# Kernel tuning notes

Hardware: AMD Instinct MI355X
Metric: run time of the kernel (lower is better)

The kernel has to match this reference:

```python
import jax, jax.numpy as jnp
import numpy as np

N_POINTS = 131072
N_SEG = 16
C = 256
BN_EPS = 1e-5


def setup_inputs() -> dict:
    key = jax.random.key(0)
    ks = jax.random.split(key, 6)
    x = jax.random.normal(ks[0], (N_POINTS, C), jnp.float32)
    # Ragged segment end-offsets (cumulative counts), strictly increasing, last == N_POINTS.
    rng = np.random.default_rng(0)
    base = N_POINTS // N_SEG
    counts = base + rng.integers(-base // 32, base // 32, N_SEG)
    counts[-1] += N_POINTS - counts.sum()
    o = jnp.asarray(np.cumsum(counts), jnp.int32)
    s1 = 1.0 / np.sqrt(2 * C)  # linear1: Linear(2C -> C)
    s2 = 1.0 / np.sqrt(C)      # linear2: Linear(C -> C)
    W1 = jax.random.uniform(ks[1], (2 * C, C), jnp.float32, -s1, s1)
    b1 = jax.random.uniform(ks[2], (C,), jnp.float32, -s1, s1)
    W2 = jax.random.uniform(ks[3], (C, C), jnp.float32, -s2, s2)
    b2 = jax.random.uniform(ks[4], (C,), jnp.float32, -s2, s2)
    gamma = jnp.ones((C,), jnp.float32)
    beta = jnp.zeros((C,), jnp.float32)
    return {"x": x, "o": o, "W1": W1, "b1": b1, "W2": W2, "b2": b2,
            "gamma": gamma, "beta": beta}


def reference(x, o, W1, b1, W2, b2, gamma, beta):
    n, c = x.shape
    s = o.shape[0]
    # segment id per point from cumulative end-offsets
    seg_id = jnp.searchsorted(o, jnp.arange(n), side="right")  # [N]
    counts = jnp.concatenate([o[:1], o[1:] - o[:-1]])          # [S]
    # per-segment mean pooling (x_b.sum(0, True) / cnt)
    sums = jax.ops.segment_sum(x, seg_id, num_segments=s)      # [S, C]
    means = sums / counts[:, None].astype(x.dtype)
    # linear2: Linear(C, C) + ReLU on segment means
    y = jax.nn.relu(means @ W2 + b2)                           # [S, C]
    # broadcast-concat back to points, then linear1: Linear(2C, C)
    h = jnp.concatenate([x, y[seg_id]], axis=1) @ W1 + b1      # [N, C]
    # BatchNorm1d (training mode: batch statistics, biased variance) + ReLU
    mu = h.mean(axis=0)
    var = h.var(axis=0)
    out = jax.nn.relu((h - mu) * (gamma / jnp.sqrt(var + BN_EPS)) + beta)
    return out
```

## Files before the change

kernel.cpp:

```cpp
#include <hip/hip_runtime.h>
#include <stdint.h>

#define N_PTS 131072
#define NC 256
#define NSEG 16
#define BN_EPSF 1e-5f

typedef __attribute__((ext_vector_type(8))) short bf16x8;
typedef __attribute__((ext_vector_type(4))) float f32x4;

__device__ __forceinline__ unsigned short f2bf(float f) {
  union { float f; uint32_t u; } v; v.f = f;
  uint32_t u = v.u;
  uint32_t r = (u + 0x7fffu + ((u >> 16) & 1u)) >> 16;
  return (unsigned short)r;
}

__device__ __forceinline__ int swz(int col, int row) {
  return (col & ~63) | ((((col >> 3) & 7) ^ (row & 7)) << 3) | (col & 7);
}

__device__ __forceinline__ void gll16(const unsigned short* g, unsigned short* l) {
  __builtin_amdgcn_global_load_lds(
      (const __attribute__((address_space(1))) void*)g,
      (__attribute__((address_space(3))) void*)l, 16, 0, 0);
}

__global__ __launch_bounds__(256) void k_prep(const float* __restrict__ W1,
                                              unsigned short* __restrict__ w1t,
                                              float* __restrict__ zerobuf) {
  int b = blockIdx.x, t = threadIdx.x;
  if (b >= 16) {
    int i = (b - 16) * 256 + t;
    if (i < 8448) zerobuf[i] = 0.f;
    return;
  }
  __shared__ float tile[64][65];
  int bx = b & 3, by = b >> 2;
  int k0 = by * 64, j0 = bx * 64;
  int r = t >> 6, c = t & 63;
#pragma unroll
  for (int i = 0; i < 16; ++i) {
    int kk = r + i * 4;
    tile[kk][c] = W1[(size_t)(k0 + kk) * NC + j0 + c];
  }
  __syncthreads();
#pragma unroll
  for (int i = 0; i < 16; ++i) {
    int jj = r + i * 4;
    int row = j0 + jj, col = k0 + c;
    w1t[(size_t)row * NC + swz(col, row)] = f2bf(tile[c][jj]);
  }
}

__global__ __launch_bounds__(256) void k_gemm1(
    const float* __restrict__ x, const int* __restrict__ o,
    const unsigned short* __restrict__ w1t,
    unsigned short* __restrict__ x_bf,
    float* __restrict__ seg_sums, float* __restrict__ hseg,
    float* __restrict__ gsumsq) {
  __shared__ __align__(16) unsigned short lA[64 * NC];
  __shared__ __align__(16) unsigned short lB[NC * 64];
  __shared__ float s_acc[2][NC];
  __shared__ float s_hA[NC], s_hB[NC], s_q[NC];
  __shared__ int o_s[NSEG];
  int t = threadIdx.x, lane = t & 63, w = t >> 6;
  int row0 = blockIdx.x * 64;
  if (t < NSEG) o_s[t] = o[t];
  s_acc[0][t] = 0.f;
  s_acc[1][t] = 0.f;
  __syncthreads();
  int c0 = lane * 4;
  int s0 = 0;
  while (o_s[s0] <= row0) ++s0;
  int e0 = o_s[s0];
  int s1 = (s0 < NSEG - 1) ? s0 + 1 : s0;

  {
    float4 accA = {0.f, 0.f, 0.f, 0.f}, accB = {0.f, 0.f, 0.f, 0.f};
    const float4* xv = (const float4*)x;
#pragma unroll
    for (int i = 0; i < 16; ++i) {
      int rl = w + i * 4;
      int r = row0 + rl;
      float4 v = xv[(size_t)r * 64 + lane];
      ushort4 b;
      b.x = f2bf(v.x); b.y = f2bf(v.y); b.z = f2bf(v.z); b.w = f2bf(v.w);
      int sc = swz(c0, r);
      *(ushort4*)(x_bf + (size_t)r * NC + sc) = b;
      *(ushort4*)(lA + rl * NC + sc) = b;
      bool inA = (r < e0);
      accA.x += inA ? v.x : 0.f; accB.x += inA ? 0.f : v.x;
      accA.y += inA ? v.y : 0.f; accB.y += inA ? 0.f : v.y;
      accA.z += inA ? v.z : 0.f; accB.z += inA ? 0.f : v.z;
      accA.w += inA ? v.w : 0.f; accB.w += inA ? 0.f : v.w;
    }
    atomicAdd(&s_acc[0][c0 + 0], accA.x);
    atomicAdd(&s_acc[0][c0 + 1], accA.y);
    atomicAdd(&s_acc[0][c0 + 2], accA.z);
    atomicAdd(&s_acc[0][c0 + 3], accA.w);
    atomicAdd(&s_acc[1][c0 + 0], accB.x);
    atomicAdd(&s_acc[1][c0 + 1], accB.y);
    atomicAdd(&s_acc[1][c0 + 2], accB.z);
    atomicAdd(&s_acc[1][c0 + 3], accB.w);
  }

  f32x4 acc[4][4] = {};
  for (int kt = 0; kt < 4; ++kt) {
#pragma unroll
    for (int i = 0; i < 8; ++i) {
      int tp = t + i * 256;
      gll16(w1t + (size_t)(tp >> 3) * NC + kt * 64 + (t & 7) * 8, lB + tp * 8);
    }
    __syncthreads();
#pragma unroll
    for (int kk = 0; kk < 2; ++kk) {
      bf16x8 af[4], bfr[4];
      int sl = kk * 4 + (lane >> 4);
#pragma unroll
      for (int mm = 0; mm < 4; ++mm) {
        int r = mm * 16 + (lane & 15);
        af[mm] = *(const bf16x8*)(lA + r * NC + kt * 64 + ((sl ^ (r & 7)) << 3));
      }
#pragma unroll
      for (int nn = 0; nn < 4; ++nn) {
        int jrow = w * 64 + nn * 16 + (lane & 15);
        bfr[nn] = *(const bf16x8*)(lB + jrow * 64 + ((sl ^ (jrow & 7)) << 3));
      }
#pragma unroll
      for (int mm = 0; mm < 4; ++mm)
#pragma unroll
        for (int nn = 0; nn < 4; ++nn)
          acc[mm][nn] = __builtin_amdgcn_mfma_f32_16x16x32_bf16(af[mm], bfr[nn],
                                                                acc[mm][nn], 0, 0, 0);
    }
    __syncthreads();
  }

  int cl = lane & 15, q = lane >> 4;
#pragma unroll
  for (int nn = 0; nn < 4; ++nn) {
    int col = w * 64 + nn * 16 + cl;
    float pA = 0.f, pB = 0.f, pq = 0.f;
#pragma unroll
    for (int mm = 0; mm < 4; ++mm) {
#pragma unroll
      for (int r_ = 0; r_ < 4; ++r_) {
        int row = row0 + mm * 16 + q * 4 + r_;
        float gv = acc[mm][nn][r_];
        bool inA = (row < e0);
        pA += inA ? gv : 0.f;
        pB += inA ? 0.f : gv;
        pq += gv * gv;
      }
    }
    pA += __shfl_xor(pA, 16, 64); pA += __shfl_xor(pA, 32, 64);
    pB += __shfl_xor(pB, 16, 64); pB += __shfl_xor(pB, 32, 64);
    pq += __shfl_xor(pq, 16, 64); pq += __shfl_xor(pq, 32, 64);
    if (q == 0) { s_hA[col] = pA; s_hB[col] = pB; s_q[col] = pq; }
  }
  __syncthreads();
  atomicAdd(&seg_sums[s0 * NC + t], s_acc[0][t]);
  atomicAdd(&seg_sums[s1 * NC + t], s_acc[1][t]);
  atomicAdd(&hseg[s0 * NC + t], s_hA[t]);
  atomicAdd(&hseg[s1 * NC + t], s_hB[t]);
  atomicAdd(&gsumsq[t], s_q[t]);
}

__global__ __launch_bounds__(256) void k_seg_mlp(
    const int* __restrict__ o, const float* __restrict__ seg_sums,
    const float* __restrict__ W1, const float* __restrict__ b1,
    const float* __restrict__ W2, const float* __restrict__ b2,
    float* __restrict__ z) {
  __shared__ float mean_s[NC];
  __shared__ float y_s[NC];
  int b = blockIdx.x, j = threadIdx.x;
  int start = (b == 0) ? 0 : o[b - 1];
  float inv = 1.f / (float)(o[b] - start);
  mean_s[j] = seg_sums[b * NC + j] * inv;
  __syncthreads();
  float a = b2[j];
  for (int k = 0; k < NC; ++k) a += mean_s[k] * W2[k * NC + j];
  y_s[j] = fmaxf(a, 0.f);
  __syncthreads();
  float a2 = b1[j];
  for (int k = 0; k < NC; ++k) a2 += y_s[k] * W1[(NC + k) * NC + j];
  z[b * NC + j] = a2;
}

__global__ __launch_bounds__(256) void k_gemm2(
    const unsigned short* __restrict__ x_bf, const unsigned short* __restrict__ w1t,
    const int* __restrict__ o, const float* __restrict__ z,
    const float* __restrict__ hseg, const float* __restrict__ gsumsq,
    const float* __restrict__ gamma, const float* __restrict__ beta,
    float* __restrict__ out) {
  __shared__ __align__(16) unsigned short lA[64 * NC];
  __shared__ __align__(16) unsigned short lB[NC * 64];
  __shared__ float s_scale[NC], s_shift[NC];
  __shared__ int o_s[NSEG];
  int t = threadIdx.x, lane = t & 63, w = t >> 6;
  int row0 = blockIdx.x * 64;
  if (t < NSEG) o_s[t] = o[t];
  __syncthreads();
  {
    float cs = 0.f, cq = gsumsq[t];
    int prev = 0;
#pragma unroll
    for (int s = 0; s < NSEG; ++s) {
      float cnt = (float)(o_s[s] - prev);
      prev = o_s[s];
      float hs = hseg[s * NC + t], zz = z[s * NC + t];
      cs += hs + cnt * zz;
      cq += (2.f * hs + cnt * zz) * zz;
    }
    float invN = 1.f / (float)N_PTS;
    float mu = cs * invN;
    float var = cq * invN - mu * mu;
    float sc = gamma[t] * rsqrtf(var + BN_EPSF);
    s_scale[t] = sc;
    s_shift[t] = beta[t] - mu * sc;
  }
#pragma unroll
  for (int i = 0; i < 8; ++i) {
    int tp = t + i * 256;
    gll16(x_bf + (size_t)(row0 + (tp >> 5)) * NC + (tp & 31) * 8, lA + tp * 8);
  }
  f32x4 acc[4][4] = {};
  for (int kt = 0; kt < 4; ++kt) {
#pragma unroll
    for (int i = 0; i < 8; ++i) {
      int tp = t + i * 256;
      gll16(w1t + (size_t)(tp >> 3) * NC + kt * 64 + (t & 7) * 8, lB + tp * 8);
    }
    __syncthreads();
#pragma unroll
    for (int kk = 0; kk < 2; ++kk) {
      bf16x8 af[4], bfr[4];
      int sl = kk * 4 + (lane >> 4);
#pragma unroll
      for (int mm = 0; mm < 4; ++mm) {
        int r = mm * 16 + (lane & 15);
        af[mm] = *(const bf16x8*)(lA + r * NC + kt * 64 + ((sl ^ (r & 7)) << 3));
      }
#pragma unroll
      for (int nn = 0; nn < 4; ++nn) {
        int jrow = w * 64 + nn * 16 + (lane & 15);
        bfr[nn] = *(const bf16x8*)(lB + jrow * 64 + ((sl ^ (jrow & 7)) << 3));
      }
#pragma unroll
      for (int mm = 0; mm < 4; ++mm)
#pragma unroll
        for (int nn = 0; nn < 4; ++nn)
          acc[mm][nn] = __builtin_amdgcn_mfma_f32_16x16x32_bf16(bfr[nn], af[mm],
                                                                acc[mm][nn], 0, 0, 0);
    }
    __syncthreads();
  }
  int s0 = 0;
  while (o_s[s0] <= row0) ++s0;
  int e0 = o_s[s0];
  int s1 = (s0 < NSEG - 1) ? s0 + 1 : s0;
  int rl = lane & 15, q = lane >> 4;
#pragma unroll
  for (int mm = 0; mm < 4; ++mm) {
    int row = row0 + mm * 16 + rl;
    int sg = (row < e0) ? s0 : s1;
#pragma unroll
    for (int nn = 0; nn < 4; ++nn) {
      int c = w * 64 + nn * 16 + q * 4;
      float4 z4 = *(const float4*)(z + sg * NC + c);
      float4 sc4 = *(const float4*)(s_scale + c);
      float4 sh4 = *(const float4*)(s_shift + c);
      float4 o4;
      o4.x = fmaxf((acc[mm][nn][0] + z4.x) * sc4.x + sh4.x, 0.f);
      o4.y = fmaxf((acc[mm][nn][1] + z4.y) * sc4.y + sh4.y, 0.f);
      o4.z = fmaxf((acc[mm][nn][2] + z4.z) * sc4.z + sh4.z, 0.f);
      o4.w = fmaxf((acc[mm][nn][3] + z4.w) * sc4.w + sh4.w, 0.f);
      *(float4*)(out + (size_t)row * NC + c) = o4;
    }
  }
}

extern "C" void kernel_launch(void* const* d_in, const int* in_sizes, int n_in,
                              void* d_out, int out_size, void* d_ws, size_t ws_size,
                              hipStream_t stream) {
  const float* x = (const float*)d_in[0];
  const int* o = (const int*)d_in[1];
  const float* W1 = (const float*)d_in[2];
  const float* b1 = (const float*)d_in[3];
  const float* W2 = (const float*)d_in[4];
  const float* b2 = (const float*)d_in[5];
  const float* gamma = (const float*)d_in[6];
  const float* beta = (const float*)d_in[7];
  float* out = (float*)d_out;

  char* ws = (char*)d_ws;
  unsigned short* x_bf = (unsigned short*)ws;
  char* base2 = ws + 67108864;
  float* seg_sums = (float*)(base2);
  float* hseg     = (float*)(base2 + 16384);
  float* gsumsq   = (float*)(base2 + 32768);
  float* z        = (float*)(base2 + 33792);
  unsigned short* w1t = (unsigned short*)(base2 + 50176);

  k_prep<<<49, 256, 0, stream>>>(W1, w1t, seg_sums);
  k_gemm1<<<2048, 256, 0, stream>>>(x, o, w1t, x_bf, seg_sums, hseg, gsumsq);
  k_seg_mlp<<<16, 256, 0, stream>>>(o, seg_sums, W1, b1, W2, b2, z);
  k_gemm2<<<2048, 256, 0, stream>>>(x_bf, w1t, o, z, hseg, gsumsq,
                                    gamma, beta, out);
}
```

Before: 346.5 us.

## Store GEMM1 result in bf16 and replace second GEMM with elementwise apply

Instead of writing bf16 x and recomputing the x@W1 GEMM in a second kernel, the first GEMM now stores its output tile as bf16 to workspace, and the final kernel only reads it back, adds the segment term and applies BatchNorm and ReLU. GEMM1 moves to 512 threads per block, with each wave covering 32 columns, and issues the first W1 k-tile load before the x conversion. This removes a whole second GEMM and its W1 tile loads, at the cost of rounding the pre-BN activation to bf16 before normalisation, which may add numerical error.

```diff
diff --git a/kernel.cpp b/kernel.cpp
--- a/kernel.cpp
+++ b/kernel.cpp
@@ -14,6 +14,9 @@
   uint32_t u = v.u;
   uint32_t r = (u + 0x7fffu + ((u >> 16) & 1u)) >> 16;
   return (unsigned short)r;
+}
+__device__ __forceinline__ float bf2f(unsigned short h) {
+  union { uint32_t u; float f; } v; v.u = ((uint32_t)h) << 16; return v.f;
 }
 
 __device__ __forceinline__ int swz(int col, int row) {
@@ -53,10 +56,10 @@
   }
 }
 
-__global__ __launch_bounds__(256) void k_gemm1(
+__global__ __launch_bounds__(512, 4) void k_gemm1(
     const float* __restrict__ x, const int* __restrict__ o,
     const unsigned short* __restrict__ w1t,
-    unsigned short* __restrict__ x_bf,
+    unsigned short* __restrict__ g_bf,
     float* __restrict__ seg_sums, float* __restrict__ hseg,
     float* __restrict__ gsumsq) {
   __shared__ __align__(16) unsigned short lA[64 * NC];
@@ -67,9 +70,15 @@
   int t = threadIdx.x, lane = t & 63, w = t >> 6;
   int row0 = blockIdx.x * 64;
   if (t < NSEG) o_s[t] = o[t];
-  s_acc[0][t] = 0.f;
-  s_acc[1][t] = 0.f;
-  __syncthreads();
+  if (t < NC) { s_acc[0][t] = 0.f; s_acc[1][t] = 0.f; }
+  __syncthreads();
+
+#pragma unroll
+  for (int i = 0; i < 4; ++i) {
+    int tp = t + i * 512;
+    gll16(w1t + (size_t)(tp >> 3) * NC + (tp & 7) * 8, lB + tp * 8);
+  }
+
   int c0 = lane * 4;
   int s0 = 0;
   while (o_s[s0] <= row0) ++s0;
@@ -80,15 +89,13 @@
     float4 accA = {0.f, 0.f, 0.f, 0.f}, accB = {0.f, 0.f, 0.f, 0.f};
     const float4* xv = (const float4*)x;
 #pragma unroll
-    for (int i = 0; i < 16; ++i) {
-      int rl = w + i * 4;
+    for (int i = 0; i < 8; ++i) {
+      int rl = w + i * 8;
       int r = row0 + rl;
       float4 v = xv[(size_t)r * 64 + lane];
       ushort4 b;
       b.x = f2bf(v.x); b.y = f2bf(v.y); b.z = f2bf(v.z); b.w = f2bf(v.w);
-      int sc = swz(c0, r);
-      *(ushort4*)(x_bf + (size_t)r * NC + sc) = b;
-      *(ushort4*)(lA + rl * NC + sc) = b;
+      *(ushort4*)(lA + rl * NC + swz(c0, rl)) = b;
       bool inA = (r < e0);
       accA.x += inA ? v.x : 0.f; accB.x += inA ? 0.f : v.x;
       accA.y += inA ? v.y : 0.f; accB.y += inA ? 0.f : v.y;
@@ -105,17 +112,19 @@
     atomicAdd(&s_acc[1][c0 + 3], accB.w);
   }
 
-  f32x4 acc[4][4] = {};
+  f32x4 acc[4][2] = {};
   for (int kt = 0; kt < 4; ++kt) {
-#pragma unroll
-    for (int i = 0; i < 8; ++i) {
-      int tp = t + i * 256;
-      gll16(w1t + (size_t)(tp >> 3) * NC + kt * 64 + (t & 7) * 8, lB + tp * 8);
+    if (kt > 0) {
+#pragma unroll
+      for (int i = 0; i < 4; ++i) {
+        int tp = t + i * 512;
+        gll16(w1t + (size_t)(tp >> 3) * NC + kt * 64 + (tp & 7) * 8, lB + tp * 8);
+      }
     }
     __syncthreads();
 #pragma unroll
     for (int kk = 0; kk < 2; ++kk) {
-      bf16x8 af[4], bfr[4];
+      bf16x8 af[4], bfr[2];
       int sl = kk * 4 + (lane >> 4);
 #pragma unroll
       for (int mm = 0; mm < 4; ++mm) {
@@ -123,48 +132,66 @@
         af[mm] = *(const bf16x8*)(lA + r * NC + kt * 64 + ((sl ^ (r & 7)) << 3));
       }
 #pragma unroll
-      for (int nn = 0; nn < 4; ++nn) {
-        int jrow = w * 64 + nn * 16 + (lane & 15);
+      for (int nn = 0; nn < 2; ++nn) {
+        int jrow = w * 32 + nn * 16 + (lane & 15);
         bfr[nn] = *(const bf16x8*)(lB + jrow * 64 + ((sl ^ (jrow & 7)) << 3));
       }
 #pragma unroll
       for (int mm = 0; mm < 4; ++mm)
 #pragma unroll
-        for (int nn = 0; nn < 4; ++nn)
-          acc[mm][nn] = __builtin_amdgcn_mfma_f32_16x16x32_bf16(af[mm], bfr[nn],
+        for (int nn = 0; nn < 2; ++nn)
+          acc[mm][nn] = __builtin_amdgcn_mfma_f32_16x16x32_bf16(bfr[nn], af[mm],
                                                                 acc[mm][nn], 0, 0, 0);
     }
     __syncthreads();
   }
 
-  int cl = lane & 15, q = lane >> 4;
-#pragma unroll
-  for (int nn = 0; nn < 4; ++nn) {
-    int col = w * 64 + nn * 16 + cl;
-    float pA = 0.f, pB = 0.f, pq = 0.f;
+  int rl = lane & 15, q = lane >> 4;
+#pragma unroll
+  for (int nn = 0; nn < 2; ++nn) {
+    float tA[4] = {0.f, 0.f, 0.f, 0.f};
+    float tB[4] = {0.f, 0.f, 0.f, 0.f};
+    float tq[4] = {0.f, 0.f, 0.f, 0.f};
 #pragma unroll
     for (int mm = 0; mm < 4; ++mm) {
-#pragma unroll
-      for (int r_ = 0; r_ < 4; ++r_) {
-        int row = row0 + mm * 16 + q * 4 + r_;
-        float gv = acc[mm][nn][r_];
-        bool inA = (row < e0);
-        pA += inA ? gv : 0.f;
-        pB += inA ? 0.f : gv;
-        pq += gv * gv;
-      }
-    }
-    pA += __shfl_xor(pA, 16, 64); pA += __shfl_xor(pA, 32, 64);
-    pB += __shfl_xor(pB, 16, 64); pB += __shfl_xor(pB, 32, 64);
-    pq += __shfl_xor(pq, 16, 64); pq += __shfl_xor(pq, 32, 64);
-    if (q == 0) { s_hA[col] = pA; s_hB[col] = pB; s_q[col] = pq; }
-  }
-  __syncthreads();
-  atomicAdd(&seg_sums[s0 * NC + t], s_acc[0][t]);
-  atomicAdd(&seg_sums[s1 * NC + t], s_acc[1][t]);
-  atomicAdd(&hseg[s0 * NC + t], s_hA[t]);
-  atomicAdd(&hseg[s1 * NC + t], s_hB[t]);
-  atomicAdd(&gsumsq[t], s_q[t]);
+      int row = row0 + mm * 16 + rl;
+      bool inA = (row < e0);
+      ushort4 b;
+#pragma unroll
+      for (int r = 0; r < 4; ++r) {
+        float gv = acc[mm][nn][r];
+        tA[r] += inA ? gv : 0.f;
+        tB[r] += inA ? 0.f : gv;
+        tq[r] += gv * gv;
+        ((unsigned short*)&b)[r] = f2bf(gv);
+      }
+      *(ushort4*)(g_bf + (size_t)row * NC + w * 32 + nn * 16 + q * 4) = b;
+    }
+#pragma unroll
+    for (int r = 0; r < 4; ++r) {
+      tA[r] += __shfl_xor(tA[r], 1, 64); tA[r] += __shfl_xor(tA[r], 2, 64);
+      tA[r] += __shfl_xor(tA[r], 4, 64); tA[r] += __shfl_xor(tA[r], 8, 64);
+      tB[r] += __shfl_xor(tB[r], 1, 64); tB[r] += __shfl_xor(tB[r], 2, 64);
+      tB[r] += __shfl_xor(tB[r], 4, 64); tB[r] += __shfl_xor(tB[r], 8, 64);
+      tq[r] += __shfl_xor(tq[r], 1, 64); tq[r] += __shfl_xor(tq[r], 2, 64);
+      tq[r] += __shfl_xor(tq[r], 4, 64); tq[r] += __shfl_xor(tq[r], 8, 64);
+    }
+    if (rl == 0) {
+#pragma unroll
+      for (int r = 0; r < 4; ++r) {
+        int col = w * 32 + nn * 16 + q * 4 + r;
+        s_hA[col] = tA[r]; s_hB[col] = tB[r]; s_q[col] = tq[r];
+      }
+    }
+  }
+  __syncthreads();
+  if (t < NC) {
+    atomicAdd(&seg_sums[s0 * NC + t], s_acc[0][t]);
+    atomicAdd(&seg_sums[s1 * NC + t], s_acc[1][t]);
+    atomicAdd(&hseg[s0 * NC + t], s_hA[t]);
+    atomicAdd(&hseg[s1 * NC + t], s_hB[t]);
+    atomicAdd(&gsumsq[t], s_q[t]);
+  }
 }
 
 __global__ __launch_bounds__(256) void k_seg_mlp(
@@ -188,17 +215,14 @@
   z[b * NC + j] = a2;
 }
 
-__global__ __launch_bounds__(256) void k_gemm2(
-    const unsigned short* __restrict__ x_bf, const unsigned short* __restrict__ w1t,
-    const int* __restrict__ o, const float* __restrict__ z,
-    const float* __restrict__ hseg, const float* __restrict__ gsumsq,
-    const float* __restrict__ gamma, const float* __restrict__ beta,
-    float* __restrict__ out) {
-  __shared__ __align__(16) unsigned short lA[64 * NC];
-  __shared__ __align__(16) unsigned short lB[NC * 64];
+__global__ __launch_bounds__(256) void k_apply(
+    const unsigned short* __restrict__ g_bf, const int* __restrict__ o,
+    const float* __restrict__ z, const float* __restrict__ hseg,
+    const float* __restrict__ gsumsq, const float* __restrict__ gamma,
+    const float* __restrict__ beta, float* __restrict__ out) {
   __shared__ float s_scale[NC], s_shift[NC];
   __shared__ int o_s[NSEG];
-  int t = threadIdx.x, lane = t & 63, w = t >> 6;
+  int t = threadIdx.x;
   int row0 = blockIdx.x * 64;
   if (t < NSEG) o_s[t] = o[t];
   __syncthreads();
@@ -220,64 +244,34 @@
     s_scale[t] = sc;
     s_shift[t] = beta[t] - mu * sc;
   }
-#pragma unroll
-  for (int i = 0; i < 8; ++i) {
-    int tp = t + i * 256;
-    gll16(x_bf + (size_t)(row0 + (tp >> 5)) * NC + (tp & 31) * 8, lA + tp * 8);
-  }
-  f32x4 acc[4][4] = {};
-  for (int kt = 0; kt < 4; ++kt) {
-#pragma unroll
-    for (int i = 0; i < 8; ++i) {
-      int tp = t + i * 256;
-      gll16(w1t + (size_t)(tp >> 3) * NC + kt * 64 + (t & 7) * 8, lB + tp * 8);
-    }
-    __syncthreads();
-#pragma unroll
-    for (int kk = 0; kk < 2; ++kk) {
-      bf16x8 af[4], bfr[4];
-      int sl = kk * 4 + (lane >> 4);
-#pragma unroll
-      for (int mm = 0; mm < 4; ++mm) {
-        int r = mm * 16 + (lane & 15);
-        af[mm] = *(const bf16x8*)(lA + r * NC + kt * 64 + ((sl ^ (r & 7)) << 3));
-      }
-#pragma unroll
-      for (int nn = 0; nn < 4; ++nn) {
-        int jrow = w * 64 + nn * 16 + (lane & 15);
-        bfr[nn] = *(const bf16x8*)(lB + jrow * 64 + ((sl ^ (jrow & 7)) << 3));
-      }
-#pragma unroll
-      for (int mm = 0; mm < 4; ++mm)
-#pragma unroll
-        for (int nn = 0; nn < 4; ++nn)
-          acc[mm][nn] = __builtin_amdgcn_mfma_f32_16x16x32_bf16(bfr[nn], af[mm],
-                                                                acc[mm][nn], 0, 0, 0);
-    }
-    __syncthreads();
-  }
+  __syncthreads();
   int s0 = 0;
   while (o_s[s0] <= row0) ++s0;
   int e0 = o_s[s0];
   int s1 = (s0 < NSEG - 1) ? s0 + 1 : s0;
-  int rl = lane & 15, q = lane >> 4;
-#pragma unroll
-  for (int mm = 0; mm < 4; ++mm) {
-    int row = row0 + mm * 16 + rl;
-    int sg = (row < e0) ? s0 : s1;
-#pragma unroll
-    for (int nn = 0; nn < 4; ++nn) {
-      int c = w * 64 + nn * 16 + q * 4;
-      float4 z4 = *(const float4*)(z + sg * NC + c);
-      float4 sc4 = *(const float4*)(s_scale + c);
-      float4 sh4 = *(const float4*)(s_shift + c);
-      float4 o4;
-      o4.x = fmaxf((acc[mm][nn][0] + z4.x) * sc4.x + sh4.x, 0.f);
-      o4.y = fmaxf((acc[mm][nn][1] + z4.y) * sc4.y + sh4.y, 0.f);
-      o4.z = fmaxf((acc[mm][nn][2] + z4.z) * sc4.z + sh4.z, 0.f);
-      o4.w = fmaxf((acc[mm][nn][3] + z4.w) * sc4.w + sh4.w, 0.f);
-      *(float4*)(out + (size_t)row * NC + c) = o4;
-    }
+  int cg = (t & 31) * 8, rsub = t >> 5;
+  float4 sc0 = *(const float4*)(s_scale + cg), sc1 = *(const float4*)(s_scale + cg + 4);
+  float4 sh0 = *(const float4*)(s_shift + cg), sh1 = *(const float4*)(s_shift + cg + 4);
+  float4 zA0 = *(const float4*)(z + s0 * NC + cg), zA1 = *(const float4*)(z + s0 * NC + cg + 4);
+  float4 zB0 = *(const float4*)(z + s1 * NC + cg), zB1 = *(const float4*)(z + s1 * NC + cg + 4);
+#pragma unroll
+  for (int i = 0; i < 8; ++i) {
+    int row = row0 + rsub + i * 8;
+    uint4 hv = *(const uint4*)(g_bf + (size_t)row * NC + cg);
+    bool inA = (row < e0);
+    float4 z0 = inA ? zA0 : zB0;
+    float4 z1 = inA ? zA1 : zB1;
+    float4 o0, o1;
+    o0.x = fmaxf((bf2f((unsigned short)(hv.x & 0xffffu)) + z0.x) * sc0.x + sh0.x, 0.f);
+    o0.y = fmaxf((bf2f((unsigned short)(hv.x >> 16)) + z0.y) * sc0.y + sh0.y, 0.f);
+    o0.z = fmaxf((bf2f((unsigned short)(hv.y & 0xffffu)) + z0.z) * sc0.z + sh0.z, 0.f);
+    o0.w = fmaxf((bf2f((unsigned short)(hv.y >> 16)) + z0.w) * sc0.w + sh0.w, 0.f);
+    o1.x = fmaxf((bf2f((unsigned short)(hv.z & 0xffffu)) + z1.x) * sc1.x + sh1.x, 0.f);
+    o1.y = fmaxf((bf2f((unsigned short)(hv.z >> 16)) + z1.y) * sc1.y + sh1.y, 0.f);
+    o1.z = fmaxf((bf2f((unsigned short)(hv.w & 0xffffu)) + z1.z) * sc1.z + sh1.z, 0.f);
+    o1.w = fmaxf((bf2f((unsigned short)(hv.w >> 16)) + z1.w) * sc1.w + sh1.w, 0.f);
+    *(float4*)(out + (size_t)row * NC + cg) = o0;
+    *(float4*)(out + (size_t)row * NC + cg + 4) = o1;
   }
 }
 
@@ -295,7 +289,7 @@
   float* out = (float*)d_out;
 
   char* ws = (char*)d_ws;
-  unsigned short* x_bf = (unsigned short*)ws;
+  unsigned short* g_bf = (unsigned short*)ws;
   char* base2 = ws + 67108864;
   float* seg_sums = (float*)(base2);
   float* hseg     = (float*)(base2 + 16384);
@@ -304,8 +298,7 @@
   unsigned short* w1t = (unsigned short*)(base2 + 50176);
 
   k_prep<<<49, 256, 0, stream>>>(W1, w1t, seg_sums);
-  k_gemm1<<<2048, 256, 0, stream>>>(x, o, w1t, x_bf, seg_sums, hseg, gsumsq);
+  k_gemm1<<<2048, 512, 0, stream>>>(x, o, w1t, g_bf, seg_sums, hseg, gsumsq);
   k_seg_mlp<<<16, 256, 0, stream>>>(o, seg_sums, W1, b1, W2, b2, z);
-  k_gemm2<<<2048, 256, 0, stream>>>(x_bf, w1t, o, z, hseg, gsumsq,
-                                    gamma, beta, out);
-}
+  k_apply<<<2048, 256, 0, stream>>>(g_bf, o, z, hseg, gsumsq, gamma, beta, out);
+}
```

Measured after the change: 346.4 us. About the same (-0.0%).
